# Kernel tuning notes

Hardware: AMD Instinct MI355X
Metric: run time of the kernel (lower is better)

## Reference

```python
import jax, jax.numpy as jnp
import numpy as np

SR = 16000
N_FFT = 512
HOP = 160
WIN = 320
N_MELS = 80
FMIN = 0.0
FMAX = 8000.0
PAD_TO = 8
BLANK = 27.0
PREEMPH = 0.97
LOG_EPS = 2.0 ** -24
STD_EPS = 1e-5


def _hz_to_mel(f):
    # Slaney mel scale (librosa default, htk=False)
    f = np.asarray(f, dtype=np.float64)
    f_sp = 200.0 / 3.0
    mels = f / f_sp
    min_log_hz = 1000.0
    min_log_mel = min_log_hz / f_sp
    logstep = np.log(6.4) / 27.0
    return np.where(f >= min_log_hz,
                    min_log_mel + np.log(np.maximum(f, 1e-10) / min_log_hz) / logstep,
                    mels)


def _mel_to_hz(m):
    m = np.asarray(m, dtype=np.float64)
    f_sp = 200.0 / 3.0
    freqs = m * f_sp
    min_log_hz = 1000.0
    min_log_mel = min_log_hz / f_sp
    logstep = np.log(6.4) / 27.0
    return np.where(m >= min_log_mel,
                    min_log_hz * np.exp(logstep * (m - min_log_mel)),
                    freqs)


def mel_filterbank():
    # librosa.filters.mel(16000, 512, n_mels=80, fmin=0, fmax=8000), slaney norm
    fftfreqs = np.linspace(0.0, SR / 2.0, 1 + N_FFT // 2)
    mel_f = _mel_to_hz(np.linspace(_hz_to_mel(FMIN), _hz_to_mel(FMAX), N_MELS + 2))
    fdiff = np.diff(mel_f)
    ramps = mel_f[:, None] - fftfreqs[None, :]
    lower = -ramps[:-2] / fdiff[:-1, None]
    upper = ramps[2:] / fdiff[1:, None]
    weights = np.maximum(0.0, np.minimum(lower, upper))
    enorm = 2.0 / (mel_f[2:N_MELS + 2] - mel_f[:N_MELS])  # slaney norm
    weights *= enorm[:, None]
    return weights.astype(np.float32)  # [80, 257]


def _window():
    # periodic hann of length 320, zero-padded to 512 (centered), as in nnAudio STFT
    n = np.arange(WIN)
    w = 0.5 - 0.5 * np.cos(2.0 * np.pi * n / WIN)
    pad = (N_FFT - WIN) // 2
    return np.pad(w, (pad, pad)).astype(np.float32)  # [512]


def setup_inputs() -> dict:
    key = jax.random.key(0)
    k1, k2 = jax.random.split(key)
    B, L = 32, 240000
    x = 0.1 * jax.random.normal(k1, (B, L), dtype=jnp.float32)
    xn = jax.random.randint(k2, (B,), 160000, L + 1, dtype=jnp.int64)
    filterbank = jnp.asarray(mel_filterbank())
    return {"x": x, "xn": xn, "filterbank": filterbank}


def reference(x, xn, filterbank):
    B, L = x.shape
    seq_len = (xn // HOP + 1).astype(jnp.int64)  # floor((L+pad-512)/160)+1, pad=512

    # pre-emphasis (eval mode: dither=0)
    y = jnp.concatenate([x[:, :1], x[:, 1:] - PREEMPH * x[:, :-1]], axis=1)

    # center=True reflect pad by n_fft//2
    y = jnp.pad(y, ((0, 0), (N_FFT // 2, N_FFT // 2)), mode="reflect")

    # frame: T = L//HOP + 1
    T = L // HOP + 1
    idx = jnp.arange(T)[:, None] * HOP + jnp.arange(N_FFT)[None, :]  # [T, 512]
    frames = y[:, idx]  # [B, T, 512]
    win = jnp.asarray(_window())
    spec = jnp.fft.rfft(frames * win, axis=-1)  # [B, T, 257] complex
    power = jnp.real(spec) ** 2 + jnp.imag(spec) ** 2  # |X|^2 (sqrt then ^2 in torch)

    mel = jnp.einsum("mf,btf->bmt", filterbank, power)  # [B, 80, T]
    logmel = jnp.log(mel + LOG_EPS)

    # ragged per-sample, per-feature mean/std (std unbiased, ddof=1) over valid frames
    valid = (jnp.arange(T)[None, :] < seq_len[:, None]).astype(logmel.dtype)  # [B, T]
    n = seq_len.astype(logmel.dtype)[:, None]  # [B, 1]
    vm = valid[:, None, :]  # [B, 1, T]
    mean = jnp.sum(logmel * vm, axis=-1) / n  # [B, 80]
    centered = (logmel - mean[..., None]) * vm
    var = jnp.sum(centered * centered, axis=-1) / (n - 1.0)
    std = jnp.sqrt(var) + STD_EPS
    out = (logmel - mean[..., None]) / std[..., None]

    # zero out invalid frames, then pad T to multiple of PAD_TO with BLANK
    out = out * vm
    pad_amt = T % PAD_TO
    if pad_amt != 0:
        out = jnp.pad(out, ((0, 0), (0, 0), (0, PAD_TO - pad_amt)),
                      constant_values=BLANK)
    return out, seq_len
```

## Files before the change

kernel.cpp:

```cpp
#include <hip/hip_runtime.h>
#include <math.h>

constexpr int BATCH = 32;
constexpr int LEN   = 240000;
constexpr int HOPS  = 160;
constexpr int T     = 1501;
constexpr int TOUT  = 1504;
constexpr int NMEL  = 80;
constexpr int NBIN  = 257;
constexpr int CMAX  = 20;
constexpr int WSTR  = 21;
constexpr float PRE     = 0.97f;
constexpr float LOG_EPS = 5.9604644775390625e-08f;
constexpr float STD_EPS = 1e-5f;
constexpr float BLANK_V = 27.0f;

constexpr size_t LOGMEL_ELTS = (size_t)BATCH * T * NMEL;

constexpr int BM    = 64;
constexpr int NSTEP = 10;
constexpr int CBLK  = 24;
constexpr int BSTR  = 40;
constexpr int ASTR  = 40;
constexpr int PSTR  = 260;

typedef __attribute__((ext_vector_type(8))) short bf16x8;
typedef __attribute__((ext_vector_type(4))) float f32x4;

__device__ __forceinline__ unsigned short f2bf(float f) {
  unsigned u = __float_as_uint(f);
  u = (u + 0x7FFFu + ((u >> 16) & 1u)) >> 16;
  return (unsigned short)u;
}
__device__ __forceinline__ int reflect_idx(int p) {
  p = p < 0 ? -p : p;
  return p >= LEN ? 2 * LEN - 2 - p : p;
}
__device__ __forceinline__ float yval(const float* xb, int p) {
  int r = reflect_idx(p);
  return (r == 0) ? xb[0] : (xb[r] - PRE * xb[r - 1]);
}
__device__ __forceinline__ int read_n(const int* xn32, int b) {
  int probe = xn32[1];
  int v = (probe == 0) ? xn32[2 * b] : xn32[b];
  return v / HOPS + 1;
}

__global__ __launch_bounds__(64) void k_prep(const float* __restrict__ fb,
                                             int* __restrict__ lc,
                                             float* __restrict__ wg,
                                             float* __restrict__ ps) {
  const int m = blockIdx.x;
  const int l = threadIdx.x;
  ps[m * 64 + l] = 0.f;
  int first = 1 << 20, last = -1;
  for (int it = 0; it < 5; ++it) {
    int f = it * 64 + l;
    float w = (f < NBIN) ? fb[m * NBIN + f] : 0.f;
    unsigned long long mk = __ballot(w != 0.f);
    if (mk) {
      int lo = __ffsll(mk) - 1;
      int hi = 63 - __clzll(mk);
      if (first > NBIN) first = it * 64 + lo;
      last = it * 64 + hi;
    }
  }
  int cnt = (last >= first) ? last - first + 1 : 0;
  if (cnt > CMAX) cnt = CMAX;
  if (first > NBIN) first = 0;
  if (l == 0) lc[m] = first | (cnt << 16);
  if (l < CMAX) wg[m * CMAX + l] = (l < cnt) ? fb[m * NBIN + first + l] : 0.f;
}

__global__ __launch_bounds__(256) void k_bmat(unsigned short* __restrict__ Bg) {
  int e = blockIdx.x * 256 + threadIdx.x;
  int s  = e >> 14;
  int n  = (e >> 5) & 511;
  int kl = e & 31;
  int j  = s * 32 + kl;
  float win = 0.5f - 0.5f * __cosf((float)j * (6.283185307179586f / 320.f));
  int bin = (n < 257) ? n : n - 256;
  int ph  = (bin * (j + 96)) & 511;
  float ang = (float)ph * (6.283185307179586f / 512.f);
  float tr  = (n < 257) ? __cosf(ang) : __sinf(ang);
  Bg[e] = f2bf(win * tr);
}

__global__ __launch_bounds__(512, 4) void k_dft(const float* __restrict__ x,
    const int* __restrict__ lc, const float* __restrict__ wg,
    const int* __restrict__ xn32, const unsigned short* __restrict__ Bg,
    float* __restrict__ logmel, float* __restrict__ ps) {
  __shared__ float swg[NMEL * WSTR];
  __shared__ int   slc[NMEL];
  __shared__ float red[2 * 4 * NMEL];
  __shared__ __align__(16) char uni[PSTR * BM * 4];

  unsigned short* Bl = (unsigned short*)uni;
  unsigned short* Al = (unsigned short*)(uni + 512 * BSTR * 2);
  float* P = (float*)uni;

  const int tid = threadIdx.x;
  const int wid = tid >> 6;
  const int l   = tid & 63;

  for (int i = tid; i < NMEL * CMAX; i += 512)
    swg[(i / CMAX) * WSTR + (i % CMAX)] = wg[i];
  if (tid < NMEL) slc[tid] = lc[tid];

  const int b  = blockIdx.x & 31;
  const int c  = blockIdx.x >> 5;
  const int t0 = c * BM;
  const float* xb = x + (size_t)b * LEN;
  const int nb = read_n(xn32, b);
  const bool slow = (c == 0) || (c == CBLK - 1);

  const int arow = tid >> 3;
  const int q7   = tid & 7;
  const int sbase = 160 * (t0 - 1);
  const uint4* Bg4 = (const uint4*)Bg;

  {
    #pragma unroll
    for (int p = 0; p < 4; ++p) {
      uint4 bv = Bg4[tid + 512 * p];
      int g = tid + 512 * p;
      *(uint4*)&Bl[(g >> 2) * BSTR + (g & 3) * 8] = bv;
    }
    int p0 = sbase + 160 * arow + 4 * q7;
    ushort4 a4;
    if (!slow) {
      const float4 xa0 = *(const float4*)(xb + p0);
      float xm0 = xb[p0 - 1];
      a4.x = f2bf(xa0.x - PRE * xm0);
      a4.y = f2bf(xa0.y - PRE * xa0.x);
      a4.z = f2bf(xa0.z - PRE * xa0.y);
      a4.w = f2bf(xa0.w - PRE * xa0.z);
    } else {
      a4.x = f2bf(yval(xb, p0));     a4.y = f2bf(yval(xb, p0 + 1));
      a4.z = f2bf(yval(xb, p0 + 2)); a4.w = f2bf(yval(xb, p0 + 3));
    }
    *(ushort4*)&Al[arow * ASTR + 4 * q7] = a4;
  }
  __syncthreads();

  f32x4 acc[4][4];
  const f32x4 zz = {0.f, 0.f, 0.f, 0.f};
  #pragma unroll
  for (int it = 0; it < 4; ++it)
    #pragma unroll
    for (int jt = 0; jt < 4; ++jt) acc[it][jt] = zz;

  for (int s = 0; s < NSTEP; ++s) {
    const bool pf = (s + 1 < NSTEP);
    float4 xa; float xm = 0.f;
    if (pf && !slow) {
      int p0 = sbase + 160 * arow + 32 * (s + 1) + 4 * q7;
      xa = *(const float4*)(xb + p0);
      xm = xb[p0 - 1];
    }
    bf16x8 af[4];
    #pragma unroll
    for (int it = 0; it < 4; ++it)
      af[it] = *(const bf16x8*)&Al[(16 * it + (l & 15)) * ASTR + (l >> 4) * 8];
    #pragma unroll
    for (int jt = 0; jt < 4; ++jt) {
      bf16x8 bfr = *(const bf16x8*)&Bl[(64 * wid + 16 * jt + (l & 15)) * BSTR + (l >> 4) * 8];
      #pragma unroll
      for (int it = 0; it < 4; ++it)
        acc[it][jt] = __builtin_amdgcn_mfma_f32_16x16x32_bf16(af[it], bfr, acc[it][jt], 0, 0, 0);
    }
    __syncthreads();
    if (pf) {
      #pragma unroll
      for (int p = 0; p < 4; ++p) {
        uint4 bv = Bg4[(s + 1) * 2048 + tid + 512 * p];
        int g = tid + 512 * p;
        *(uint4*)&Bl[(g >> 2) * BSTR + (g & 3) * 8] = bv;
      }
      ushort4 a4;
      if (!slow) {
        a4.x = f2bf(xa.x - PRE * xm);
        a4.y = f2bf(xa.y - PRE * xa.x);
        a4.z = f2bf(xa.z - PRE * xa.y);
        a4.w = f2bf(xa.w - PRE * xa.z);
      } else {
        int p0 = sbase + 160 * arow + 32 * (s + 1) + 4 * q7;
        a4.x = f2bf(yval(xb, p0));     a4.y = f2bf(yval(xb, p0 + 1));
        a4.z = f2bf(yval(xb, p0 + 2)); a4.w = f2bf(yval(xb, p0 + 3));
      }
      *(ushort4*)&Al[arow * ASTR + 4 * q7] = a4;
      __syncthreads();
    }
  }
  __syncthreads();

  #pragma unroll
  for (int it = 0; it < 4; ++it) {
    int fr = 16 * it + (l >> 4) * 4;
    #pragma unroll
    for (int jt = 0; jt < 4; ++jt) {
      int col = 64 * wid + 16 * jt + (l & 15);
      if (col <= 256) {
        #pragma unroll
        for (int r = 0; r < 4; ++r) {
          float v = acc[it][jt][r];
          P[(fr + r) * PSTR + col] = v * v;
        }
      }
    }
  }
  __syncthreads();
  #pragma unroll
  for (int it = 0; it < 4; ++it) {
    int fr = 16 * it + (l >> 4) * 4;
    #pragma unroll
    for (int jt = 0; jt < 4; ++jt) {
      int col = 64 * wid + 16 * jt + (l & 15);
      if (col >= 257) {
        int bin = col - 256;
        #pragma unroll
        for (int r = 0; r < 4; ++r) {
          float v = acc[it][jt][r];
          P[(fr + r) * PSTR + bin] += v * v;
        }
      }
    }
  }
  __syncthreads();

  const size_t lbase = ((size_t)b * T + t0) * NMEL;
  if (tid < 320) {
    int m = tid % 80, fc = tid / 80;
    int lo = slc[m] & 0xffff;
    const float* pw = &swg[m * WSTR];
    float lS = 0.f, lQ = 0.f;
    for (int ff = 0; ff < 16; ++ff) {
      int f = fc * 16 + ff;
      const float* pp = &P[f * PSTR + lo];
      float a_ = 0.f;
      #pragma unroll
      for (int j = 0; j < CMAX; ++j) a_ += pp[j] * pw[j];
      float lv = __logf(a_ + LOG_EPS);
      int t = t0 + f;
      if (t < T) logmel[lbase + (size_t)f * NMEL + m] = lv;
      if (t < nb) { lS += lv; lQ += lv * lv; }
    }
    red[fc * 80 + m] = lS;
    red[320 + fc * 80 + m] = lQ;
  }
  __syncthreads();
  if (tid < NMEL) {
    float S = red[tid] + red[80 + tid] + red[160 + tid] + red[240 + tid];
    float Q = red[320 + tid] + red[400 + tid] + red[480 + tid] + red[560 + tid];
    atomicAdd(&ps[b * 160 + tid], S);
    atomicAdd(&ps[b * 160 + 80 + tid], Q);
  }
}

__global__ __launch_bounds__(256) void k_apply(const float* __restrict__ logmel,
    const float* __restrict__ ps, const int* __restrict__ xn32,
    float* __restrict__ out, float* __restrict__ outseq) {
  const int bid = blockIdx.x;
  const int b = bid / 24, c = bid % 24;
  const int tbase = c * 64;
  __shared__ float tile[64 * 81];
  __shared__ float smean[80], sistd[80];
  const int tid = threadIdx.x;
  const int n = read_n(xn32, b);
  if (tid < 80) {
    float S = ps[b * 160 + tid], S2 = ps[b * 160 + 80 + tid];
    float fn = (float)n;
    float mean = S / fn;
    float var = (S2 - fn * mean * mean) / (fn - 1.f);
    var = var < 0.f ? 0.f : var;
    smean[tid] = mean;
    sistd[tid] = 1.f / (sqrtf(var) + STD_EPS);
  }
  __syncthreads();

  for (int e = tid; e < 1280; e += 256) {
    int tt = e / 20, v = e % 20;
    int t = tbase + tt;
    int m0 = 4 * v;
    float4 val;
    if (t >= T)      val = make_float4(BLANK_V, BLANK_V, BLANK_V, BLANK_V);
    else if (t >= n) val = make_float4(0.f, 0.f, 0.f, 0.f);
    else {
      const float4 g = *(const float4*)&logmel[((size_t)b * T + t) * NMEL + m0];
      val.x = (g.x - smean[m0])     * sistd[m0];
      val.y = (g.y - smean[m0 + 1]) * sistd[m0 + 1];
      val.z = (g.z - smean[m0 + 2]) * sistd[m0 + 2];
      val.w = (g.w - smean[m0 + 3]) * sistd[m0 + 3];
    }
    float* tp = &tile[tt * 81 + m0];
    tp[0] = val.x; tp[1] = val.y; tp[2] = val.z; tp[3] = val.w;
  }
  __syncthreads();
  for (int e = tid; e < 1280; e += 256) {
    int m = e >> 4, v = e & 15;
    int tt0 = 4 * v;
    int t = tbase + tt0;
    if (t < TOUT) {
      float4 o;
      o.x = tile[(tt0    ) * 81 + m];
      o.y = tile[(tt0 + 1) * 81 + m];
      o.z = tile[(tt0 + 2) * 81 + m];
      o.w = tile[(tt0 + 3) * 81 + m];
      *(float4*)&out[((size_t)b * NMEL + m) * TOUT + t] = o;
    }
  }
  if (c == 0 && tid == 0) outseq[b] = (float)n;
}

extern "C" void kernel_launch(void* const* d_in, const int* in_sizes, int n_in,
                              void* d_out, int out_size, void* d_ws, size_t ws_size,
                              hipStream_t stream) {
  const float* x  = (const float*)d_in[0];
  const int*   xn = (const int*)d_in[1];
  const float* fb = (const float*)d_in[2];

  float* out    = (float*)d_out;
  float* outseq = out + (size_t)BATCH * NMEL * TOUT;

  float* logmel = (float*)d_ws;
  int*   lc = (int*)(logmel + LOGMEL_ELTS);
  float* wg = (float*)(lc + NMEL);
  float* ps = wg + NMEL * CMAX;
  unsigned short* Bg = (unsigned short*)(ps + 32 * 160);

  k_prep <<<NMEL, 64, 0, stream>>>(fb, lc, wg, ps);
  k_bmat <<<640, 256, 0, stream>>>(Bg);
  k_dft  <<<BATCH * CBLK, 512, 0, stream>>>(x, lc, wg, xn, Bg, logmel, ps);
  k_apply<<<BATCH * CBLK, 256, 0, stream>>>(logmel, ps, xn, out, outseq);
}
```

Baseline: 138.2 us.

## Load DFT basis fragments directly from global memory and double-buffer A tile

The DFT basis matrix is now written pre-swizzled in MFMA fragment order, so each wave loads its B fragments straight from global memory (L2-resident) instead of staging them through LDS. The A (pre-emphasized frame) tile is double-buffered in LDS, which cuts the loop to one barrier per step. The filterbank prep and basis-generation kernels are merged into one launch. The trade-off is more global and L2 traffic per block, since every block rereads the full basis, in exchange for less LDS traffic and fewer barriers.

After: 128.2 us. 7.2% less time.

```diff
diff --git a/kernel.cpp b/kernel.cpp
--- a/kernel.cpp
+++ b/kernel.cpp
@@ -20,7 +20,6 @@
 constexpr int BM    = 64;
 constexpr int NSTEP = 10;
 constexpr int CBLK  = 24;
-constexpr int BSTR  = 40;
 constexpr int ASTR  = 40;
 constexpr int PSTR  = 260;
 
@@ -46,57 +45,61 @@
   return v / HOPS + 1;
 }
 
-__global__ __launch_bounds__(64) void k_prep(const float* __restrict__ fb,
-                                             int* __restrict__ lc,
-                                             float* __restrict__ wg,
-                                             float* __restrict__ ps) {
-  const int m = blockIdx.x;
-  const int l = threadIdx.x;
-  ps[m * 64 + l] = 0.f;
-  int first = 1 << 20, last = -1;
-  for (int it = 0; it < 5; ++it) {
-    int f = it * 64 + l;
-    float w = (f < NBIN) ? fb[m * NBIN + f] : 0.f;
-    unsigned long long mk = __ballot(w != 0.f);
-    if (mk) {
-      int lo = __ffsll(mk) - 1;
-      int hi = 63 - __clzll(mk);
-      if (first > NBIN) first = it * 64 + lo;
-      last = it * 64 + hi;
-    }
-  }
-  int cnt = (last >= first) ? last - first + 1 : 0;
-  if (cnt > CMAX) cnt = CMAX;
-  if (first > NBIN) first = 0;
-  if (l == 0) lc[m] = first | (cnt << 16);
-  if (l < CMAX) wg[m * CMAX + l] = (l < cnt) ? fb[m * NBIN + first + l] : 0.f;
-}
-
-__global__ __launch_bounds__(256) void k_bmat(unsigned short* __restrict__ Bg) {
-  int e = blockIdx.x * 256 + threadIdx.x;
-  int s  = e >> 14;
-  int n  = (e >> 5) & 511;
-  int kl = e & 31;
-  int j  = s * 32 + kl;
-  float win = 0.5f - 0.5f * __cosf((float)j * (6.283185307179586f / 320.f));
-  int bin = (n < 257) ? n : n - 256;
-  int ph  = (bin * (j + 96)) & 511;
-  float ang = (float)ph * (6.283185307179586f / 512.f);
-  float tr  = (n < 257) ? __cosf(ang) : __sinf(ang);
-  Bg[e] = f2bf(win * tr);
+__global__ __launch_bounds__(256) void k_setup(const float* __restrict__ fb,
+                                               int* __restrict__ lc,
+                                               float* __restrict__ wg,
+                                               float* __restrict__ ps,
+                                               unsigned short* __restrict__ Bf) {
+  if (blockIdx.x < 80) {
+    const int m = blockIdx.x;
+    const int l = threadIdx.x;
+    if (l < 64) {
+      ps[m * 64 + l] = 0.f;
+      int first = 1 << 20, last = -1;
+      for (int it = 0; it < 5; ++it) {
+        int f = it * 64 + l;
+        float w = (f < NBIN) ? fb[m * NBIN + f] : 0.f;
+        unsigned long long mk = __ballot(w != 0.f);
+        if (mk) {
+          int lo = __ffsll(mk) - 1;
+          int hi = 63 - __clzll(mk);
+          if (first > NBIN) first = it * 64 + lo;
+          last = it * 64 + hi;
+        }
+      }
+      int cnt = (last >= first) ? last - first + 1 : 0;
+      if (cnt > CMAX) cnt = CMAX;
+      if (first > NBIN) first = 0;
+      if (l == 0) lc[m] = first | (cnt << 16);
+      if (l < CMAX) wg[m * CMAX + l] = (l < cnt) ? fb[m * NBIN + first + l] : 0.f;
+    }
+  } else {
+    int e = (blockIdx.x - 80) * 256 + threadIdx.x;
+    int d  = e & 7;
+    int l  = (e >> 3) & 63;
+    int rg = (e >> 9) & 31;
+    int s  = e >> 14;
+    int n  = 16 * rg + (l & 15);
+    int j  = 32 * s + 8 * (l >> 4) + d;
+    float win = 0.5f - 0.5f * __cosf((float)j * (6.283185307179586f / 320.f));
+    int bin = (n < 257) ? n : n - 256;
+    int ph  = (bin * (j + 96)) & 511;
+    float ang = (float)ph * (6.283185307179586f / 512.f);
+    float tr  = (n < 257) ? __cosf(ang) : __sinf(ang);
+    Bf[e] = f2bf(win * tr);
+  }
 }
 
 __global__ __launch_bounds__(512, 4) void k_dft(const float* __restrict__ x,
     const int* __restrict__ lc, const float* __restrict__ wg,
-    const int* __restrict__ xn32, const unsigned short* __restrict__ Bg,
+    const int* __restrict__ xn32, const unsigned short* __restrict__ Bf,
     float* __restrict__ logmel, float* __restrict__ ps) {
   __shared__ float swg[NMEL * WSTR];
   __shared__ int   slc[NMEL];
   __shared__ float red[2 * 4 * NMEL];
   __shared__ __align__(16) char uni[PSTR * BM * 4];
 
-  unsigned short* Bl = (unsigned short*)uni;
-  unsigned short* Al = (unsigned short*)(uni + 512 * BSTR * 2);
+  unsigned short* Al = (unsigned short*)uni;
   float* P = (float*)uni;
 
   const int tid = threadIdx.x;
@@ -117,15 +120,9 @@
   const int arow = tid >> 3;
   const int q7   = tid & 7;
   const int sbase = 160 * (t0 - 1);
-  const uint4* Bg4 = (const uint4*)Bg;
+  const bf16x8* Bf8 = (const bf16x8*)Bf;
 
   {
-    #pragma unroll
-    for (int p = 0; p < 4; ++p) {
-      uint4 bv = Bg4[tid + 512 * p];
-      int g = tid + 512 * p;
-      *(uint4*)&Bl[(g >> 2) * BSTR + (g & 3) * 8] = bv;
-    }
     int p0 = sbase + 160 * arow + 4 * q7;
     ushort4 a4;
     if (!slow) {
@@ -152,31 +149,25 @@
 
   for (int s = 0; s < NSTEP; ++s) {
     const bool pf = (s + 1 < NSTEP);
+    bf16x8 bfr[4];
+    #pragma unroll
+    for (int jt = 0; jt < 4; ++jt)
+      bfr[jt] = Bf8[(s * 32 + 4 * wid + jt) * 64 + l];
     float4 xa; float xm = 0.f;
     if (pf && !slow) {
       int p0 = sbase + 160 * arow + 32 * (s + 1) + 4 * q7;
       xa = *(const float4*)(xb + p0);
       xm = xb[p0 - 1];
     }
-    bf16x8 af[4];
-    #pragma unroll
-    for (int it = 0; it < 4; ++it)
-      af[it] = *(const bf16x8*)&Al[(16 * it + (l & 15)) * ASTR + (l >> 4) * 8];
-    #pragma unroll
-    for (int jt = 0; jt < 4; ++jt) {
-      bf16x8 bfr = *(const bf16x8*)&Bl[(64 * wid + 16 * jt + (l & 15)) * BSTR + (l >> 4) * 8];
+    const unsigned short* Ab = Al + (s & 1) * (BM * ASTR);
+    #pragma unroll
+    for (int it = 0; it < 4; ++it) {
+      bf16x8 af = *(const bf16x8*)&Ab[(16 * it + (l & 15)) * ASTR + (l >> 4) * 8];
       #pragma unroll
-      for (int it = 0; it < 4; ++it)
-        acc[it][jt] = __builtin_amdgcn_mfma_f32_16x16x32_bf16(af[it], bfr, acc[it][jt], 0, 0, 0);
-    }
-    __syncthreads();
+      for (int jt = 0; jt < 4; ++jt)
+        acc[it][jt] = __builtin_amdgcn_mfma_f32_16x16x32_bf16(af, bfr[jt], acc[it][jt], 0, 0, 0);
+    }
     if (pf) {
-      #pragma unroll
-      for (int p = 0; p < 4; ++p) {
-        uint4 bv = Bg4[(s + 1) * 2048 + tid + 512 * p];
-        int g = tid + 512 * p;
-        *(uint4*)&Bl[(g >> 2) * BSTR + (g & 3) * 8] = bv;
-      }
       ushort4 a4;
       if (!slow) {
         a4.x = f2bf(xa.x - PRE * xm);
@@ -188,11 +179,10 @@
         a4.x = f2bf(yval(xb, p0));     a4.y = f2bf(yval(xb, p0 + 1));
         a4.z = f2bf(yval(xb, p0 + 2)); a4.w = f2bf(yval(xb, p0 + 3));
       }
-      *(ushort4*)&Al[arow * ASTR + 4 * q7] = a4;
-      __syncthreads();
-    }
-  }
-  __syncthreads();
+      *(ushort4*)&Al[((s + 1) & 1) * (BM * ASTR) + arow * ASTR + 4 * q7] = a4;
+    }
+    __syncthreads();
+  }
 
   #pragma unroll
   for (int it = 0; it < 4; ++it) {
@@ -326,10 +316,9 @@
   int*   lc = (int*)(logmel + LOGMEL_ELTS);
   float* wg = (float*)(lc + NMEL);
   float* ps = wg + NMEL * CMAX;
-  unsigned short* Bg = (unsigned short*)(ps + 32 * 160);
-
-  k_prep <<<NMEL, 64, 0, stream>>>(fb, lc, wg, ps);
-  k_bmat <<<640, 256, 0, stream>>>(Bg);
-  k_dft  <<<BATCH * CBLK, 512, 0, stream>>>(x, lc, wg, xn, Bg, logmel, ps);
+  unsigned short* Bf = (unsigned short*)(ps + 32 * 160);
+
+  k_setup<<<720, 256, 0, stream>>>(fb, lc, wg, ps, Bf);
+  k_dft  <<<BATCH * CBLK, 512, 0, stream>>>(x, lc, wg, xn, Bf, logmel, ps);
   k_apply<<<BATCH * CBLK, 256, 0, stream>>>(logmel, ps, xn, out, outseq);
 }
```
